# Kernel optimization log

Measured on AMD Instinct MI355X. Metric: run time of the kernel, lower is better.

Reference implementation:

```python
import jax, jax.numpy as jnp
import numpy as np

N_EMBED = 1024
N_HEAD = 16
HEAD_SIZE = N_EMBED // N_HEAD  # 64
SEQ = 2048
BATCH = 2
EPS = 1e-5


def setup_inputs() -> dict:
    key = jax.random.key(0)
    ks = jax.random.split(key, 16)
    s = lambda fan_in: 1.0 / np.sqrt(fan_in)
    d, h, hs, f = N_EMBED, N_HEAD, HEAD_SIZE, 4 * N_EMBED
    return {
        "x": jax.random.normal(ks[0], (BATCH, SEQ, d), dtype=jnp.float32),
        # per-head QKV projections (no bias), stacked over heads: [H, D, hs]
        "wq": jax.random.normal(ks[1], (h, d, hs), dtype=jnp.float32) * s(d),
        "wk": jax.random.normal(ks[2], (h, d, hs), dtype=jnp.float32) * s(d),
        "wv": jax.random.normal(ks[3], (h, d, hs), dtype=jnp.float32) * s(d),
        "w_proj": jax.random.normal(ks[4], (d, d), dtype=jnp.float32) * s(d),
        "b_proj": jnp.zeros((d,), dtype=jnp.float32),
        "w1": jax.random.normal(ks[5], (d, f), dtype=jnp.float32) * s(d),
        "b1": jnp.zeros((f,), dtype=jnp.float32),
        "w2": jax.random.normal(ks[6], (f, d), dtype=jnp.float32) * s(f),
        "b2": jnp.zeros((d,), dtype=jnp.float32),
        "g1": jnp.ones((d,), dtype=jnp.float32),
        "be1": jnp.zeros((d,), dtype=jnp.float32),
        "g2": jnp.ones((d,), dtype=jnp.float32),
        "be2": jnp.zeros((d,), dtype=jnp.float32),
    }


def _layer_norm(x, gamma, beta):
    mu = jnp.mean(x, axis=-1, keepdims=True)
    var = jnp.mean(jnp.square(x - mu), axis=-1, keepdims=True)
    return (x - mu) * jax.lax.rsqrt(var + EPS) * gamma + beta


def reference(x, wq, wk, wv, w_proj, b_proj, w1, b1, w2, b2, g1, be1, g2, be2):
    B, S, D = x.shape
    # per-head projections (vectorized over heads): [B, H, S, hs]
    q = jnp.einsum("bsd,hdk->bhsk", x, wq)
    k = jnp.einsum("bsd,hdk->bhsk", x, wk)
    v = jnp.einsum("bsd,hdk->bhsk", x, wv)
    scale = HEAD_SIZE ** -0.5
    scores = jnp.einsum("bhsk,bhtk->bhst", q, k) * scale  # [B,H,S,S]
    causal = jnp.tril(jnp.ones((S, S), dtype=bool))
    scores = jnp.where(causal, scores, -jnp.inf)
    w = jax.nn.softmax(scores, axis=-1)  # dropout=0 -> identity
    attn = jnp.einsum("bhst,bhtk->bhsk", w, v)  # [B,H,S,hs]
    # concat heads (head-major ordering matches torch.cat over heads)
    attn = attn.transpose(0, 2, 1, 3).reshape(B, S, D)
    y = attn @ w_proj + b_proj
    x = _layer_norm(x + y, g1, be1)
    y = jax.nn.relu(x @ w1 + b1) @ w2 + b2
    x = _layer_norm(x + y, g2, be2)
    return x
```

## Files before the change

### kernel.cpp

```cpp
#include <hip/hip_runtime.h>


typedef unsigned short u16;
typedef unsigned int u32;
typedef __attribute__((ext_vector_type(8))) short bf16x8;
typedef __attribute__((ext_vector_type(4))) float f32x4;
typedef __attribute__((ext_vector_type(2))) u32 u32x2;
typedef __attribute__((ext_vector_type(4))) _Float16 f16x4;

#define MFMA16(a, b, c) __builtin_amdgcn_mfma_f32_16x16x32_bf16(a, b, c, 0, 0, 0)
#define MFMAH(a, b, c) __builtin_amdgcn_mfma_f32_16x16x16f16(a, b, c, 0, 0, 0)

__device__ __forceinline__ u16 f2b(float f) {
  unsigned int u = __builtin_bit_cast(unsigned int, f);
  u = (u + 0x7fffu + ((u >> 16) & 1u)) >> 16;
  return (u16)u;
}

__device__ __forceinline__ void gload_lds16(const u16* g, u16* l) {
  __builtin_amdgcn_global_load_lds((const __attribute__((address_space(1))) void*)g,
                                   (__attribute__((address_space(3))) void*)l, 16, 0, 0);
}

__device__ __forceinline__ u32 pkrtz(float lo, float hi) {
  return __builtin_bit_cast(u32, __builtin_amdgcn_cvt_pkrtz(lo, hi));
}

__device__ __forceinline__ f16x4 pack4h(float a, float b, float c, float d) {
  u32x2 r = {pkrtz(a, b), pkrtz(c, d)};
  return __builtin_bit_cast(f16x4, r);
}


__global__ __launch_bounds__(256) void castx_kernel(const float* __restrict__ src,
                                                    u16* __restrict__ dst) {
  int i = (blockIdx.x * 256 + threadIdx.x) * 4;
  float4 v = *(const float4*)(src + i);
  dst[i + 0] = f2b(v.x);
  dst[i + 1] = f2b(v.y);
  dst[i + 2] = f2b(v.z);
  dst[i + 3] = f2b(v.w);
}

__global__ __launch_bounds__(256) void tcast_kernel(const float* __restrict__ src,
                                                    u16* __restrict__ dst, int R, int C) {
  __shared__ float tile[32][33];
  int tx = threadIdx.x, ty = threadIdx.y;
  int r0 = blockIdx.y * 32, c0 = blockIdx.x * 32;
#pragma unroll
  for (int i = 0; i < 4; ++i)
    tile[ty + i * 8][tx] = src[(size_t)(r0 + ty + i * 8) * C + c0 + tx];
  __syncthreads();
#pragma unroll
  for (int i = 0; i < 4; ++i)
    dst[(size_t)(c0 + ty + i * 8) * R + r0 + tx] = f2b(tile[tx][ty + i * 8]);
}

__global__ __launch_bounds__(256) void tcast_qkv_kernel(const float* __restrict__ wq,
                                                        const float* __restrict__ wk,
                                                        const float* __restrict__ wv,
                                                        u16* __restrict__ dst) {
  __shared__ float tile[32][33];
  int tx = threadIdx.x, ty = threadIdx.y;
  int z = blockIdx.z;
  int p = z >> 4, h = z & 15;
  const float* src = (p == 0 ? wq : (p == 1 ? wk : wv)) + (size_t)h * 1024 * 64;
  float scale = (p == 0) ? 0.1803368801f : 1.0f;
  u16* dbase = dst + (size_t)(p * 1024 + h * 64) * 1024;
  int r0 = blockIdx.y * 32, c0 = blockIdx.x * 32;
#pragma unroll
  for (int i = 0; i < 4; ++i)
    tile[ty + i * 8][tx] = src[(size_t)(r0 + ty + i * 8) * 64 + c0 + tx];
  __syncthreads();
#pragma unroll
  for (int i = 0; i < 4; ++i)
    dbase[(size_t)(c0 + ty + i * 8) * 1024 + r0 + tx] = f2b(tile[tx][ty + i * 8] * scale);
}


template <int MODE, int BN>
__global__ __launch_bounds__(256) void gemm_bf16(const u16* __restrict__ A,
                                                 const u16* __restrict__ Bt, int M, int N,
                                                 int K, const float* __restrict__ bias,
                                                 const float* __restrict__ resid,
                                                 u16* __restrict__ outB,
                                                 float* __restrict__ outF, int ldc,
                                                 u16* __restrict__ vtg) {
  constexpr int BM = 128, BK = 64;
  constexpr int IM = (BN == 128) ? 4 : 2;
  constexpr int JN = 4;
  __shared__ u16 As[BM * BK];
  __shared__ u16 Bs[BN * BK];
  int t = threadIdx.x;
  int m0 = blockIdx.y * BM, n0 = blockIdx.x * BN;
  int lane = t & 63, wid = t >> 6;
  int wm = (BN == 128) ? (wid >> 1) * 64 : wid * 32;
  int wn = (BN == 128) ? (wid & 1) * 64 : 0;
  int m16 = lane & 15, quad = lane >> 4;
  int sw = m16 & 7;

  f32x4 acc[IM][JN] = {};

  for (int k0 = 0; k0 < K; k0 += BK) {
    __syncthreads();
#pragma unroll
    for (int i = 0; i < 4; ++i) {
      int S = i * 256 + t;
      int row = S >> 3, c = S & 7;
      gload_lds16(&A[(size_t)(m0 + row) * K + k0 + (c ^ (row & 7)) * 8],
                  &As[(i * 256 + wid * 64) * 8]);
    }
#pragma unroll
    for (int i = 0; i < BN / 32; ++i) {
      int S = i * 256 + t;
      int row = S >> 3, c = S & 7;
      gload_lds16(&Bt[(size_t)(n0 + row) * K + k0 + (c ^ (row & 7)) * 8],
                  &Bs[(i * 256 + wid * 64) * 8]);
    }
    __syncthreads();
#pragma unroll
    for (int kk = 0; kk < 2; ++kk) {
      bf16x8 af[IM], bfr[JN];
      int slot = (kk * 4 + quad) ^ sw;
#pragma unroll
      for (int i = 0; i < IM; ++i)
        af[i] = *(const bf16x8*)&As[(wm + i * 16 + m16) * BK + slot * 8];
#pragma unroll
      for (int j = 0; j < JN; ++j)
        bfr[j] = *(const bf16x8*)&Bs[(wn + j * 16 + m16) * BK + slot * 8];
#pragma unroll
      for (int i = 0; i < IM; ++i)
#pragma unroll
        for (int j = 0; j < JN; ++j) acc[i][j] = MFMA16(af[i], bfr[j], acc[i][j]);
    }
  }

  if (MODE == 3 && n0 >= 2048) {
#pragma unroll
    for (int i = 0; i < IM; ++i)
#pragma unroll
      for (int j = 0; j < JN; ++j) {
        int dg = n0 + wn + j * 16 + m16 - 2048;
        int hh = dg >> 6, dd = dg & 63;
        int token = m0 + wm + i * 16 + quad * 4;
        int bb = token >> 11, tt = token & 2047;
        u32x2 pv = {pkrtz(acc[i][j][0], acc[i][j][1]),
                    pkrtz(acc[i][j][2], acc[i][j][3])};
        *(u32x2*)&vtg[(((size_t)bb * 16 + hh) * 64 + dd) * 2048 + tt] = pv;
      }
    return;
  }

#pragma unroll
  for (int i = 0; i < IM; ++i)
#pragma unroll
    for (int j = 0; j < JN; ++j) {
      int col = n0 + wn + j * 16 + m16;
      float bv = (MODE == 0 || MODE == 3) ? 0.0f : bias[col];
#pragma unroll
      for (int r = 0; r < 4; ++r) {
        int row = m0 + wm + i * 16 + quad * 4 + r;
        float v = acc[i][j][r];
        if (MODE == 1 || MODE == 2) v += bv;
        if (MODE == 1) v = v > 0.0f ? v : 0.0f;
        if (MODE == 2) {
          v += resid[(size_t)row * ldc + col];
          outF[(size_t)row * ldc + col] = v;
        } else {
          outB[(size_t)row * ldc + col] = f2b(v);
        }
      }
    }
}


__constant__ unsigned char SLOT_LPT[40] = {
    3, 4, 6, 8, 10, 11, 12, 13, 15, 16, 18, 19, 21, 22, 23, 24, 25, 26, 28, 29,
    30, 32, 33, 34, 36, 37, 38, 39,
    2, 9, 20, 35,
    1, 7, 17, 31,
    0, 5, 14, 27};
__constant__ unsigned char SLOT_QB[40] = {0, 1, 2, 3, 4, 4, 5, 5, 6, 6, 7, 7, 8, 8,
                                          8, 9, 9, 9, 10, 10, 10, 11, 11, 11, 12, 12,
                                          12, 12, 13, 13, 13, 13, 14, 14, 14, 14, 15,
                                          15, 15, 15};
__constant__ unsigned char SLOT_S[40] = {0, 0, 0, 0, 0, 1, 0, 1, 0, 1, 0, 1, 0, 1,
                                         2, 0, 1, 2, 0, 1, 2, 0, 1, 2, 0, 1, 2, 3,
                                         0, 1, 2, 3, 0, 1, 2, 3, 0, 1, 2, 3};
__constant__ unsigned char QB_BASE[16] = {0, 1, 2, 3, 4, 6, 8, 10,
                                          12, 15, 18, 21, 24, 28, 32, 36};

__global__ __launch_bounds__(256) void attn_part(const u16* __restrict__ qk,
                                                 const u16* __restrict__ vtg,
                                                 u16* __restrict__ opart,
                                                 float2* __restrict__ ml) {
  int rank = blockIdx.x >> 5, bh = blockIdx.x & 31;
  int slot = SLOT_LPT[rank];
  int qb = SLOT_QB[slot], s = SLOT_S[slot];
  int b = bh >> 4, h = bh & 15;
  int nseg = (qb >> 2) + 1;
  int k_start = s * 512;
  int k_end = min((s + 1) * 512, (qb + 1) * 128);
  int iters = (k_end - k_start) >> 6;

  int t = threadIdx.x, lane = t & 63, w = t >> 6;
  int m16 = lane & 15, quad = lane >> 4;
  int wq0 = qb * 128 + w * 32;

  __shared__ u16 Ks[2][64 * 64];
  __shared__ u16 Vs[2][64 * 64];

  bf16x8 qa[2][2];
#pragma unroll
  for (int qs = 0; qs < 2; ++qs) {
    const u16* qp = qk + (size_t)(b * 2048 + wq0 + qs * 16 + m16) * 2048 + h * 64;
    qa[qs][0] = *(const bf16x8*)&qp[quad * 8];
    qa[qs][1] = *(const bf16x8*)&qp[32 + quad * 8];
  }

  f32x4 oT[2][4] = {};
  f32x4 lacc[2] = {};
  float mrun[2] = {-1e30f, -1e30f};

  int row0 = t >> 3, c0 = t & 7;
  int row1 = 32 + row0;
  const u16* kbase = qk + (size_t)(b * 2048) * 2048 + 1024 + h * 64;
  const u16* vbase = vtg + ((size_t)(b * 16 + h) * 64) * 2048;
  int sw = m16 & 7;

#define STAGE_ASYNC(T0, BUF)                                                        \
  {                                                                                 \
    gload_lds16(&kbase[(size_t)((T0) + row0) * 2048 + (c0 ^ (row0 & 7)) * 8],       \
                &Ks[BUF][(w * 64) * 8]);                                            \
    gload_lds16(&kbase[(size_t)((T0) + row1) * 2048 + (c0 ^ (row1 & 7)) * 8],       \
                &Ks[BUF][(256 + w * 64) * 8]);                                      \
    gload_lds16(&vbase[(size_t)row0 * 2048 + (T0) + (c0 ^ (row0 & 7)) * 8],         \
                &Vs[BUF][(w * 64) * 8]);                                            \
    gload_lds16(&vbase[(size_t)row1 * 2048 + (T0) + (c0 ^ (row1 & 7)) * 8],         \
                &Vs[BUF][(256 + w * 64) * 8]);                                      \
  }

  STAGE_ASYNC(k_start, 0);
  __syncthreads();

  for (int it = 0; it < iters; ++it) {
    int t0 = k_start + it * 64;
    int cur = it & 1;
    if (it + 1 < iters) STAGE_ASYNC(t0 + 64, !cur);

    if (t0 <= wq0 + 31) {
      f32x4 sv[2][4];
#pragma unroll
      for (int ts = 0; ts < 4; ++ts) {
        bf16x8 ka0 = *(const bf16x8*)&Ks[cur][(ts * 16 + m16) * 64 + (quad ^ sw) * 8];
        bf16x8 ka1 =
            *(const bf16x8*)&Ks[cur][(ts * 16 + m16) * 64 + ((4 + quad) ^ sw) * 8];
#pragma unroll
        for (int qs = 0; qs < 2; ++qs) {
          f32x4 a = {};
          a = MFMA16(ka0, qa[qs][0], a);
          a = MFMA16(ka1, qa[qs][1], a);
          sv[qs][ts] = a;
        }
      }
      if (t0 + 63 > wq0) {
#pragma unroll
        for (int qs = 0; qs < 2; ++qs)
#pragma unroll
          for (int ts = 0; ts < 4; ++ts)
#pragma unroll
            for (int rr = 0; rr < 4; ++rr) {
              int key = t0 + ts * 16 + quad * 4 + rr;
              if (key > wq0 + qs * 16 + m16) sv[qs][ts][rr] = -3e38f;
            }
      }
#pragma unroll
      for (int qs = 0; qs < 2; ++qs) {
        float mx = fmaxf(fmaxf(sv[qs][0][0], sv[qs][0][1]),
                         fmaxf(sv[qs][0][2], sv[qs][0][3]));
#pragma unroll
        for (int ts = 1; ts < 4; ++ts)
          mx = fmaxf(mx, fmaxf(fmaxf(sv[qs][ts][0], sv[qs][ts][1]),
                               fmaxf(sv[qs][ts][2], sv[qs][ts][3])));
        mx = fmaxf(mx, __shfl_xor(mx, 16));
        mx = fmaxf(mx, __shfl_xor(mx, 32));
        float mnew = fmaxf(mrun[qs], mx);
        float alpha = exp2f(mrun[qs] - mnew);
        mrun[qs] = mnew;
        lacc[qs] *= alpha;
#pragma unroll
        for (int ds = 0; ds < 4; ++ds) oT[qs][ds] *= alpha;
      }
      f16x4 pf[2][4];
#pragma unroll
      for (int qs = 0; qs < 2; ++qs)
#pragma unroll
        for (int ts = 0; ts < 4; ++ts) {
          float p0 = exp2f(sv[qs][ts][0] - mrun[qs]);
          float p1 = exp2f(sv[qs][ts][1] - mrun[qs]);
          float p2 = exp2f(sv[qs][ts][2] - mrun[qs]);
          float p3 = exp2f(sv[qs][ts][3] - mrun[qs]);
          lacc[qs][0] += p0;
          lacc[qs][1] += p1;
          lacc[qs][2] += p2;
          lacc[qs][3] += p3;
          pf[qs][ts] = pack4h(p0, p1, p2, p3);
        }
#pragma unroll
      for (int ts = 0; ts < 4; ++ts)
#pragma unroll
        for (int ds = 0; ds < 4; ++ds) {
          f16x4 av = __builtin_bit_cast(
              f16x4, *(const u32x2*)&Vs[cur][(ds * 16 + m16) * 64 +
                                             (((ts * 2 + (quad >> 1)) ^ sw) * 8) +
                                             (quad & 1) * 4]);
          oT[0][ds] = MFMAH(av, pf[0][ts], oT[0][ds]);
          oT[1][ds] = MFMAH(av, pf[1][ts], oT[1][ds]);
        }
    }
    __syncthreads();
  }
#undef STAGE_ASYNC

  size_t sbase = ((size_t)bh * 40 + slot) * 128;
#pragma unroll
  for (int qs = 0; qs < 2; ++qs) {
    float ls = lacc[qs][0] + lacc[qs][1] + lacc[qs][2] + lacc[qs][3];
    ls += __shfl_xor(ls, 16);
    ls += __shfl_xor(ls, 32);
    int qloc = w * 32 + qs * 16 + m16;
#pragma unroll
    for (int ds = 0; ds < 4; ++ds) {
      f32x4 o = oT[qs][ds];
      u32x2 ov = {pkrtz(o[0], o[1]), pkrtz(o[2], o[3])};
      *(u32x2*)&opart[(sbase + qloc) * 64 + ds * 16 + quad * 4] = ov;
    }
    if (quad == 0) ml[sbase + qloc] = make_float2(mrun[qs], ls);
  }
}

__global__ __launch_bounds__(256) void attn_comb(const u16* __restrict__ opart,
                                                 const float2* __restrict__ ml,
                                                 u16* __restrict__ attn_out) {
  int qb = blockIdx.x, bh = blockIdx.y;
  int b = bh >> 4, h = bh & 15;
  int nseg = (qb >> 2) + 1;
  int base = QB_BASE[qb];
  int t = threadIdx.x;
  int q = t >> 1, dh = (t & 1) * 32;

  float m[4], l[4], wgt[4];
  float M = -3e38f;
  for (int s = 0; s < nseg; ++s) {
    float2 v = ml[((size_t)bh * 40 + base + s) * 128 + q];
    m[s] = v.x;
    l[s] = v.y;
    M = fmaxf(M, v.x);
  }
  float lsum = 0.0f;
  for (int s = 0; s < nseg; ++s) {
    wgt[s] = exp2f(m[s] - M);
    lsum += wgt[s] * l[s];
  }
  float rl = 1.0f / lsum;

  size_t orow = (size_t)(b * 2048 + qb * 128 + q) * 1024 + h * 64 + dh;
#pragma unroll 2
  for (int dd = 0; dd < 32; dd += 4) {
    float o0 = 0, o1 = 0, o2 = 0, o3 = 0;
    for (int s = 0; s < nseg; ++s) {
      f16x4 hv = __builtin_bit_cast(
          f16x4,
          *(const u32x2*)&opart[(((size_t)bh * 40 + base + s) * 128 + q) * 64 + dh + dd]);
      o0 += wgt[s] * (float)hv[0];
      o1 += wgt[s] * (float)hv[1];
      o2 += wgt[s] * (float)hv[2];
      o3 += wgt[s] * (float)hv[3];
    }
    u32x2 ov = {(u32)f2b(o0 * rl) | ((u32)f2b(o1 * rl) << 16),
                (u32)f2b(o2 * rl) | ((u32)f2b(o3 * rl) << 16)};
    *(u32x2*)&attn_out[orow + dd] = ov;
  }
}


__global__ __launch_bounds__(256) void ln_kernel(const float* __restrict__ in,
                                                 const float* __restrict__ g,
                                                 const float* __restrict__ be,
                                                 float* __restrict__ outF,
                                                 u16* __restrict__ outB) {
  int row = blockIdx.x;
  int t = threadIdx.x;
  const float* p = in + (size_t)row * 1024 + t * 4;
  float4 v = *(const float4*)p;
  float s = v.x + v.y + v.z + v.w;
  float sq = v.x * v.x + v.y * v.y + v.z * v.z + v.w * v.w;
#pragma unroll
  for (int d = 1; d < 64; d <<= 1) {
    s += __shfl_xor(s, d);
    sq += __shfl_xor(sq, d);
  }
  __shared__ float red[8];
  int lane = t & 63, wid = t >> 6;
  if (lane == 0) {
    red[wid] = s;
    red[4 + wid] = sq;
  }
  __syncthreads();
  s = red[0] + red[1] + red[2] + red[3];
  sq = red[4] + red[5] + red[6] + red[7];
  float mu = s * (1.0f / 1024.0f);
  float var = sq * (1.0f / 1024.0f) - mu * mu;
  float rstd = rsqrtf(var + 1e-5f);
  float4 gv = *(const float4*)(g + t * 4);
  float4 bv = *(const float4*)(be + t * 4);
  float o0 = (v.x - mu) * rstd * gv.x + bv.x;
  float o1 = (v.y - mu) * rstd * gv.y + bv.y;
  float o2 = (v.z - mu) * rstd * gv.z + bv.z;
  float o3 = (v.w - mu) * rstd * gv.w + bv.w;
  size_t o = (size_t)row * 1024 + t * 4;
  if (outF) {
    float4 ov = {o0, o1, o2, o3};
    *(float4*)(outF + o) = ov;
  }
  if (outB) {
    outB[o + 0] = f2b(o0);
    outB[o + 1] = f2b(o1);
    outB[o + 2] = f2b(o2);
    outB[o + 3] = f2b(o3);
  }
}


extern "C" void kernel_launch(void* const* d_in, const int* in_sizes, int n_in,
                              void* d_out, int out_size, void* d_ws, size_t ws_size,
                              hipStream_t stream) {
  const float* x = (const float*)d_in[0];
  const float* wq = (const float*)d_in[1];
  const float* wk = (const float*)d_in[2];
  const float* wv = (const float*)d_in[3];
  const float* w_proj = (const float*)d_in[4];
  const float* b_proj = (const float*)d_in[5];
  const float* w1 = (const float*)d_in[6];
  const float* b1 = (const float*)d_in[7];
  const float* w2 = (const float*)d_in[8];
  const float* b2 = (const float*)d_in[9];
  const float* g1 = (const float*)d_in[10];
  const float* be1 = (const float*)d_in[11];
  const float* g2 = (const float*)d_in[12];
  const float* be2 = (const float*)d_in[13];
  float* out = (float*)d_out;

  const int M = 4096;
  char* w = (char*)d_ws;
  u16* Xbf = (u16*)w;        w += (size_t)M * 1024 * 2;
  u16* WqkvT = (u16*)w;      w += (size_t)3072 * 1024 * 2;
  u16* WprojT = (u16*)w;     w += (size_t)1024 * 1024 * 2;
  u16* W1T = (u16*)w;        w += (size_t)4096 * 1024 * 2;
  u16* W2T = (u16*)w;        w += (size_t)1024 * 4096 * 2;
  u16* QK = (u16*)w;         w += (size_t)M * 2048 * 2;
  u16* Vtg = (u16*)w;        w += (size_t)2 * 16 * 64 * 2048 * 2;
  u16* Attn = (u16*)w;       w += (size_t)M * 1024 * 2;
  float* X1f = (float*)w;    w += (size_t)M * 1024 * 4;
  u16* X1b = (u16*)w;        w += (size_t)M * 1024 * 2;
  u16* Hbuf = QK;
  u16* Opart = (u16*)X1f;
  float2* Ml = (float2*)((char*)X1f + (size_t)1280 * 8192 * 2);

  castx_kernel<<<M * 1024 / 1024, 256, 0, stream>>>(x, Xbf);
  tcast_qkv_kernel<<<dim3(2, 32, 48), dim3(32, 8), 0, stream>>>(wq, wk, wv, WqkvT);
  tcast_kernel<<<dim3(32, 32), dim3(32, 8), 0, stream>>>(w_proj, WprojT, 1024, 1024);
  tcast_kernel<<<dim3(128, 32), dim3(32, 8), 0, stream>>>(w1, W1T, 1024, 4096);
  tcast_kernel<<<dim3(32, 128), dim3(32, 8), 0, stream>>>(w2, W2T, 4096, 1024);

  gemm_bf16<3, 128><<<dim3(3072 / 128, M / 128), 256, 0, stream>>>(
      Xbf, WqkvT, M, 3072, 1024, nullptr, nullptr, QK, nullptr, 2048, Vtg);

  attn_part<<<1280, 256, 0, stream>>>(QK, Vtg, Opart, Ml);
  attn_comb<<<dim3(16, 32), 256, 0, stream>>>(Opart, Ml, Attn);

  gemm_bf16<2, 64><<<dim3(1024 / 64, M / 128), 256, 0, stream>>>(
      Attn, WprojT, M, 1024, 1024, b_proj, x, nullptr, out, 1024, nullptr);

  ln_kernel<<<M, 256, 0, stream>>>(out, g1, be1, X1f, X1b);

  gemm_bf16<1, 128><<<dim3(4096 / 128, M / 128), 256, 0, stream>>>(
      X1b, W1T, M, 4096, 1024, b1, nullptr, Hbuf, nullptr, 4096, nullptr);

  gemm_bf16<2, 64><<<dim3(1024 / 64, M / 128), 256, 0, stream>>>(
      Hbuf, W2T, M, 1024, 4096, b2, X1f, nullptr, out, 1024, nullptr);

  ln_kernel<<<M, 256, 0, stream>>>(out, g2, be2, out, nullptr);
}
```

Measured before the change: 370.3 us.

## Split-K output GEMMs with fused LN reduction and rebalanced attention split schedule

The projection and FFN-down GEMMs now use 128x128 tiles with split-K (2 and 4 slices). Each slice writes fp16 partials, and a new ln_comb kernel sums them with the bias and residual before applying layernorm. This replaces the narrower BN=64 tiles and the separate residual epilogue. The attention partition table is redone so query blocks up to 7 write normalized output directly and only the later blocks use split partials combined by a smaller attn_comb. Block index order is also swapped so M is the fastest-varying dimension. In exchange, partial buffers add memory traffic and the fp16 partials add rounding error.

```diff
diff --git a/kernel.cpp b/kernel.cpp
--- a/kernel.cpp
+++ b/kernel.cpp
@@ -29,6 +29,10 @@
 __device__ __forceinline__ f16x4 pack4h(float a, float b, float c, float d) {
   u32x2 r = {pkrtz(a, b), pkrtz(c, d)};
   return __builtin_bit_cast(f16x4, r);
+}
+
+__device__ __forceinline__ u16 f2h(float v) {
+  return __builtin_bit_cast(u16, (_Float16)v);
 }
 
 
@@ -78,43 +82,41 @@
 }
 
 
-template <int MODE, int BN>
+template <int MODE>
 __global__ __launch_bounds__(256) void gemm_bf16(const u16* __restrict__ A,
                                                  const u16* __restrict__ Bt, int M, int N,
-                                                 int K, const float* __restrict__ bias,
-                                                 const float* __restrict__ resid,
-                                                 u16* __restrict__ outB,
-                                                 float* __restrict__ outF, int ldc,
+                                                 int Kc, int lda,
+                                                 const float* __restrict__ bias,
+                                                 u16* __restrict__ outB, int ldc,
                                                  u16* __restrict__ vtg) {
-  constexpr int BM = 128, BK = 64;
-  constexpr int IM = (BN == 128) ? 4 : 2;
-  constexpr int JN = 4;
+  constexpr int BM = 128, BN = 128, BK = 64;
+  constexpr int IM = 4, JN = 4;
   __shared__ u16 As[BM * BK];
   __shared__ u16 Bs[BN * BK];
   int t = threadIdx.x;
-  int m0 = blockIdx.y * BM, n0 = blockIdx.x * BN;
+  int m0 = blockIdx.x * BM, n0 = blockIdx.y * BN;
+  int kb = blockIdx.z * Kc;
   int lane = t & 63, wid = t >> 6;
-  int wm = (BN == 128) ? (wid >> 1) * 64 : wid * 32;
-  int wn = (BN == 128) ? (wid & 1) * 64 : 0;
+  int wm = (wid >> 1) * 64, wn = (wid & 1) * 64;
   int m16 = lane & 15, quad = lane >> 4;
   int sw = m16 & 7;
 
   f32x4 acc[IM][JN] = {};
 
-  for (int k0 = 0; k0 < K; k0 += BK) {
+  for (int k0 = kb; k0 < kb + Kc; k0 += BK) {
     __syncthreads();
 #pragma unroll
     for (int i = 0; i < 4; ++i) {
       int S = i * 256 + t;
       int row = S >> 3, c = S & 7;
-      gload_lds16(&A[(size_t)(m0 + row) * K + k0 + (c ^ (row & 7)) * 8],
+      gload_lds16(&A[(size_t)(m0 + row) * lda + k0 + (c ^ (row & 7)) * 8],
                   &As[(i * 256 + wid * 64) * 8]);
     }
 #pragma unroll
-    for (int i = 0; i < BN / 32; ++i) {
+    for (int i = 0; i < 4; ++i) {
       int S = i * 256 + t;
       int row = S >> 3, c = S & 7;
-      gload_lds16(&Bt[(size_t)(n0 + row) * K + k0 + (c ^ (row & 7)) * 8],
+      gload_lds16(&Bt[(size_t)(n0 + row) * lda + k0 + (c ^ (row & 7)) * 8],
                   &Bs[(i * 256 + wid * 64) * 8]);
     }
     __syncthreads();
@@ -151,57 +153,56 @@
     return;
   }
 
+  u16* pb = (MODE == 4) ? outB + (size_t)blockIdx.z * M * N : outB;
 #pragma unroll
   for (int i = 0; i < IM; ++i)
 #pragma unroll
     for (int j = 0; j < JN; ++j) {
       int col = n0 + wn + j * 16 + m16;
-      float bv = (MODE == 0 || MODE == 3) ? 0.0f : bias[col];
+      float bv = (MODE == 1) ? bias[col] : 0.0f;
 #pragma unroll
       for (int r = 0; r < 4; ++r) {
         int row = m0 + wm + i * 16 + quad * 4 + r;
         float v = acc[i][j][r];
-        if (MODE == 1 || MODE == 2) v += bv;
-        if (MODE == 1) v = v > 0.0f ? v : 0.0f;
-        if (MODE == 2) {
-          v += resid[(size_t)row * ldc + col];
-          outF[(size_t)row * ldc + col] = v;
+        if (MODE == 1) {
+          v += bv;
+          v = v > 0.0f ? v : 0.0f;
+          pb[(size_t)row * ldc + col] = f2b(v);
+        } else if (MODE == 4) {
+          pb[(size_t)row * ldc + col] = f2h(v);
         } else {
-          outB[(size_t)row * ldc + col] = f2b(v);
+          pb[(size_t)row * ldc + col] = f2b(v);
         }
       }
     }
 }
 
 
-__constant__ unsigned char SLOT_LPT[40] = {
-    3, 4, 6, 8, 10, 11, 12, 13, 15, 16, 18, 19, 21, 22, 23, 24, 25, 26, 28, 29,
-    30, 32, 33, 34, 36, 37, 38, 39,
-    2, 9, 20, 35,
-    1, 7, 17, 31,
-    0, 5, 14, 27};
-__constant__ unsigned char SLOT_QB[40] = {0, 1, 2, 3, 4, 4, 5, 5, 6, 6, 7, 7, 8, 8,
-                                          8, 9, 9, 9, 10, 10, 10, 11, 11, 11, 12, 12,
-                                          12, 12, 13, 13, 13, 13, 14, 14, 14, 14, 15,
-                                          15, 15, 15};
-__constant__ unsigned char SLOT_S[40] = {0, 0, 0, 0, 0, 1, 0, 1, 0, 1, 0, 1, 0, 1,
-                                         2, 0, 1, 2, 0, 1, 2, 0, 1, 2, 0, 1, 2, 3,
-                                         0, 1, 2, 3, 0, 1, 2, 3, 0, 1, 2, 3};
-__constant__ unsigned char QB_BASE[16] = {0, 1, 2, 3, 4, 6, 8, 10,
-                                          12, 15, 18, 21, 24, 28, 32, 36};
+__constant__ unsigned char R_QB[32] = {7, 6, 11, 11, 5, 10, 10, 9, 9, 4, 8,
+                                       8, 3, 15, 15, 15, 15, 14, 14, 14, 13, 13,
+                                       13, 13, 12, 12, 12, 2, 14, 12, 1, 0};
+__constant__ unsigned char R_K0[32] = {0, 0, 0, 12, 0, 0, 11, 0, 10, 0, 0,
+                                       9, 0, 0, 8, 16, 24, 0, 8, 16, 0, 7,
+                                       14, 21, 0, 7, 14, 0, 24, 21, 0, 0};
+__constant__ unsigned char R_NIT[32] = {16, 14, 12, 12, 12, 11, 11, 10, 10, 10, 9,
+                                        9, 8, 8, 8, 8, 8, 8, 8, 8, 7, 7,
+                                        7, 7, 7, 7, 7, 6, 6, 5, 4, 2};
+__constant__ unsigned char R_ST[32] = {255, 255, 6, 7, 255, 4, 5, 2, 3, 255, 0,
+                                       1, 255, 20, 21, 22, 23, 16, 17, 18, 12, 13,
+                                       14, 15, 8, 9, 10, 255, 19, 11, 255, 255};
+__constant__ unsigned char CB_BASE[8] = {0, 2, 4, 6, 8, 12, 16, 20};
 
 __global__ __launch_bounds__(256) void attn_part(const u16* __restrict__ qk,
                                                  const u16* __restrict__ vtg,
+                                                 u16* __restrict__ attn_out,
                                                  u16* __restrict__ opart,
                                                  float2* __restrict__ ml) {
   int rank = blockIdx.x >> 5, bh = blockIdx.x & 31;
-  int slot = SLOT_LPT[rank];
-  int qb = SLOT_QB[slot], s = SLOT_S[slot];
+  int qb = R_QB[rank];
+  int k_start = R_K0[rank] * 64;
+  int iters = R_NIT[rank];
+  int st = R_ST[rank];
   int b = bh >> 4, h = bh & 15;
-  int nseg = (qb >> 2) + 1;
-  int k_start = s * 512;
-  int k_end = min((s + 1) * 512, (qb + 1) * 128);
-  int iters = (k_end - k_start) >> 6;
 
   int t = threadIdx.x, lane = t & 63, w = t >> 6;
   int m16 = lane & 15, quad = lane >> 4;
@@ -322,37 +323,56 @@
   }
 #undef STAGE_ASYNC
 
-  size_t sbase = ((size_t)bh * 40 + slot) * 128;
-#pragma unroll
-  for (int qs = 0; qs < 2; ++qs) {
-    float ls = lacc[qs][0] + lacc[qs][1] + lacc[qs][2] + lacc[qs][3];
-    ls += __shfl_xor(ls, 16);
-    ls += __shfl_xor(ls, 32);
-    int qloc = w * 32 + qs * 16 + m16;
-#pragma unroll
-    for (int ds = 0; ds < 4; ++ds) {
-      f32x4 o = oT[qs][ds];
-      u32x2 ov = {pkrtz(o[0], o[1]), pkrtz(o[2], o[3])};
-      *(u32x2*)&opart[(sbase + qloc) * 64 + ds * 16 + quad * 4] = ov;
-    }
-    if (quad == 0) ml[sbase + qloc] = make_float2(mrun[qs], ls);
+  if (st == 255) {
+#pragma unroll
+    for (int qs = 0; qs < 2; ++qs) {
+      float ls = lacc[qs][0] + lacc[qs][1] + lacc[qs][2] + lacc[qs][3];
+      ls += __shfl_xor(ls, 16);
+      ls += __shfl_xor(ls, 32);
+      float rl = 1.0f / ls;
+      int q = wq0 + qs * 16 + m16;
+#pragma unroll
+      for (int ds = 0; ds < 4; ++ds) {
+        f32x4 o = oT[qs][ds];
+        u32x2 ov = {(u32)f2b(o[0] * rl) | ((u32)f2b(o[1] * rl) << 16),
+                    (u32)f2b(o[2] * rl) | ((u32)f2b(o[3] * rl) << 16)};
+        *(u32x2*)&attn_out[(size_t)(b * 2048 + q) * 1024 + h * 64 + ds * 16 +
+                           quad * 4] = ov;
+      }
+    }
+  } else {
+    size_t sbase = ((size_t)st * 32 + bh) * 128;
+#pragma unroll
+    for (int qs = 0; qs < 2; ++qs) {
+      float ls = lacc[qs][0] + lacc[qs][1] + lacc[qs][2] + lacc[qs][3];
+      ls += __shfl_xor(ls, 16);
+      ls += __shfl_xor(ls, 32);
+      int qloc = w * 32 + qs * 16 + m16;
+#pragma unroll
+      for (int ds = 0; ds < 4; ++ds) {
+        f32x4 o = oT[qs][ds];
+        u32x2 ov = {pkrtz(o[0], o[1]), pkrtz(o[2], o[3])};
+        *(u32x2*)&opart[(sbase + qloc) * 64 + ds * 16 + quad * 4] = ov;
+      }
+      if (quad == 0) ml[sbase + qloc] = make_float2(mrun[qs], ls);
+    }
   }
 }
 
 __global__ __launch_bounds__(256) void attn_comb(const u16* __restrict__ opart,
                                                  const float2* __restrict__ ml,
                                                  u16* __restrict__ attn_out) {
-  int qb = blockIdx.x, bh = blockIdx.y;
+  int qb = 8 + blockIdx.x, bh = blockIdx.y;
   int b = bh >> 4, h = bh & 15;
-  int nseg = (qb >> 2) + 1;
-  int base = QB_BASE[qb];
+  int nseg = (qb < 12) ? 2 : 4;
+  int base = CB_BASE[qb - 8];
   int t = threadIdx.x;
   int q = t >> 1, dh = (t & 1) * 32;
 
   float m[4], l[4], wgt[4];
   float M = -3e38f;
   for (int s = 0; s < nseg; ++s) {
-    float2 v = ml[((size_t)bh * 40 + base + s) * 128 + q];
+    float2 v = ml[((size_t)(base + s) * 32 + bh) * 128 + q];
     m[s] = v.x;
     l[s] = v.y;
     M = fmaxf(M, v.x);
@@ -370,8 +390,8 @@
     float o0 = 0, o1 = 0, o2 = 0, o3 = 0;
     for (int s = 0; s < nseg; ++s) {
       f16x4 hv = __builtin_bit_cast(
-          f16x4,
-          *(const u32x2*)&opart[(((size_t)bh * 40 + base + s) * 128 + q) * 64 + dh + dd]);
+          f16x4, *(const u32x2*)&opart[(((size_t)(base + s) * 32 + bh) * 128 + q) * 64 +
+                                       dh + dd]);
       o0 += wgt[s] * (float)hv[0];
       o1 += wgt[s] * (float)hv[1];
       o2 += wgt[s] * (float)hv[2];
@@ -384,17 +404,34 @@
 }
 
 
-__global__ __launch_bounds__(256) void ln_kernel(const float* __restrict__ in,
-                                                 const float* __restrict__ g,
-                                                 const float* __restrict__ be,
-                                                 float* __restrict__ outF,
-                                                 u16* __restrict__ outB) {
+__global__ __launch_bounds__(256) void ln_comb(const u16* __restrict__ parts, int np,
+                                               const float* __restrict__ bias,
+                                               const float* __restrict__ resid,
+                                               const float* __restrict__ g,
+                                               const float* __restrict__ be,
+                                               float* __restrict__ outF,
+                                               u16* __restrict__ outB) {
   int row = blockIdx.x;
   int t = threadIdx.x;
-  const float* p = in + (size_t)row * 1024 + t * 4;
-  float4 v = *(const float4*)p;
-  float s = v.x + v.y + v.z + v.w;
-  float sq = v.x * v.x + v.y * v.y + v.z * v.z + v.w * v.w;
+  size_t off = (size_t)row * 1024 + t * 4;
+  float4 bv4 = *(const float4*)(bias + t * 4);
+  float a0 = bv4.x, a1 = bv4.y, a2 = bv4.z, a3 = bv4.w;
+  for (int c = 0; c < np; ++c) {
+    f16x4 hv =
+        __builtin_bit_cast(f16x4, *(const u32x2*)&parts[(size_t)c * 4096 * 1024 + off]);
+    a0 += (float)hv[0];
+    a1 += (float)hv[1];
+    a2 += (float)hv[2];
+    a3 += (float)hv[3];
+  }
+  float4 rv = *(const float4*)(resid + off);
+  a0 += rv.x;
+  a1 += rv.y;
+  a2 += rv.z;
+  a3 += rv.w;
+
+  float s = a0 + a1 + a2 + a3;
+  float sq = a0 * a0 + a1 * a1 + a2 * a2 + a3 * a3;
 #pragma unroll
   for (int d = 1; d < 64; d <<= 1) {
     s += __shfl_xor(s, d);
@@ -413,21 +450,20 @@
   float var = sq * (1.0f / 1024.0f) - mu * mu;
   float rstd = rsqrtf(var + 1e-5f);
   float4 gv = *(const float4*)(g + t * 4);
-  float4 bv = *(const float4*)(be + t * 4);
-  float o0 = (v.x - mu) * rstd * gv.x + bv.x;
-  float o1 = (v.y - mu) * rstd * gv.y + bv.y;
-  float o2 = (v.z - mu) * rstd * gv.z + bv.z;
-  float o3 = (v.w - mu) * rstd * gv.w + bv.w;
-  size_t o = (size_t)row * 1024 + t * 4;
+  float4 bev = *(const float4*)(be + t * 4);
+  float o0 = (a0 - mu) * rstd * gv.x + bev.x;
+  float o1 = (a1 - mu) * rstd * gv.y + bev.y;
+  float o2 = (a2 - mu) * rstd * gv.z + bev.z;
+  float o3 = (a3 - mu) * rstd * gv.w + bev.w;
   if (outF) {
     float4 ov = {o0, o1, o2, o3};
-    *(float4*)(outF + o) = ov;
+    *(float4*)(outF + off) = ov;
   }
   if (outB) {
-    outB[o + 0] = f2b(o0);
-    outB[o + 1] = f2b(o1);
-    outB[o + 2] = f2b(o2);
-    outB[o + 3] = f2b(o3);
+    outB[off + 0] = f2b(o0);
+    outB[off + 1] = f2b(o1);
+    outB[off + 2] = f2b(o2);
+    outB[off + 3] = f2b(o3);
   }
 }
 
@@ -457,15 +493,18 @@
   u16* WqkvT = (u16*)w;      w += (size_t)3072 * 1024 * 2;
   u16* WprojT = (u16*)w;     w += (size_t)1024 * 1024 * 2;
   u16* W1T = (u16*)w;        w += (size_t)4096 * 1024 * 2;
+  u16* X1b = (u16*)w;        w += (size_t)M * 1024 * 2;
   u16* W2T = (u16*)w;        w += (size_t)1024 * 4096 * 2;
   u16* QK = (u16*)w;         w += (size_t)M * 2048 * 2;
   u16* Vtg = (u16*)w;        w += (size_t)2 * 16 * 64 * 2048 * 2;
   u16* Attn = (u16*)w;       w += (size_t)M * 1024 * 2;
   float* X1f = (float*)w;    w += (size_t)M * 1024 * 4;
-  u16* X1b = (u16*)w;        w += (size_t)M * 1024 * 2;
+
+  u16* Pdown = Xbf;
+  u16* Pproj = QK;
   u16* Hbuf = QK;
   u16* Opart = (u16*)X1f;
-  float2* Ml = (float2*)((char*)X1f + (size_t)1280 * 8192 * 2);
+  float2* Ml = (float2*)((char*)X1f + (size_t)13 * 1024 * 1024);
 
   castx_kernel<<<M * 1024 / 1024, 256, 0, stream>>>(x, Xbf);
   tcast_qkv_kernel<<<dim3(2, 32, 48), dim3(32, 8), 0, stream>>>(wq, wk, wv, WqkvT);
@@ -473,22 +512,20 @@
   tcast_kernel<<<dim3(128, 32), dim3(32, 8), 0, stream>>>(w1, W1T, 1024, 4096);
   tcast_kernel<<<dim3(32, 128), dim3(32, 8), 0, stream>>>(w2, W2T, 4096, 1024);
 
-  gemm_bf16<3, 128><<<dim3(3072 / 128, M / 128), 256, 0, stream>>>(
-      Xbf, WqkvT, M, 3072, 1024, nullptr, nullptr, QK, nullptr, 2048, Vtg);
-
-  attn_part<<<1280, 256, 0, stream>>>(QK, Vtg, Opart, Ml);
-  attn_comb<<<dim3(16, 32), 256, 0, stream>>>(Opart, Ml, Attn);
-
-  gemm_bf16<2, 64><<<dim3(1024 / 64, M / 128), 256, 0, stream>>>(
-      Attn, WprojT, M, 1024, 1024, b_proj, x, nullptr, out, 1024, nullptr);
-
-  ln_kernel<<<M, 256, 0, stream>>>(out, g1, be1, X1f, X1b);
-
-  gemm_bf16<1, 128><<<dim3(4096 / 128, M / 128), 256, 0, stream>>>(
-      X1b, W1T, M, 4096, 1024, b1, nullptr, Hbuf, nullptr, 4096, nullptr);
-
-  gemm_bf16<2, 64><<<dim3(1024 / 64, M / 128), 256, 0, stream>>>(
-      Hbuf, W2T, M, 1024, 4096, b2, X1f, nullptr, out, 1024, nullptr);
-
-  ln_kernel<<<M, 256, 0, stream>>>(out, g2, be2, out, nullptr);
-}
+  gemm_bf16<3><<<dim3(32, 24, 1), 256, 0, stream>>>(Xbf, WqkvT, M, 3072, 1024, 1024,
+                                                    nullptr, QK, 2048, Vtg);
+
+  attn_part<<<1024, 256, 0, stream>>>(QK, Vtg, Attn, Opart, Ml);
+  attn_comb<<<dim3(8, 32), 256, 0, stream>>>(Opart, Ml, Attn);
+
+  gemm_bf16<4><<<dim3(32, 8, 2), 256, 0, stream>>>(Attn, WprojT, M, 1024, 512, 1024,
+                                                   nullptr, Pproj, 1024, nullptr);
+  ln_comb<<<M, 256, 0, stream>>>(Pproj, 2, b_proj, x, g1, be1, X1f, X1b);
+
+  gemm_bf16<1><<<dim3(32, 32, 1), 256, 0, stream>>>(X1b, W1T, M, 4096, 1024, 1024, b1,
+                                                    Hbuf, 4096, nullptr);
+
+  gemm_bf16<4><<<dim3(32, 8, 4), 256, 0, stream>>>(Hbuf, W2T, M, 1024, 1024, 4096,
+                                                   nullptr, Pdown, 1024, nullptr);
+  ln_comb<<<M, 256, 0, stream>>>(Pdown, 4, b2, X1f, g2, be2, out, nullptr);
+}
```

Result: no change. 363.4 us (-1.9%).
